# Optimization experiments

Hardware: AMD Instinct MI355X
Metric: run time of the kernel (lower is better)

Reference implementation:

```python
import jax, jax.numpy as jnp
import numpy as np

NEG_CAUSAL = -1e10  # matches torch buffer triu(ones*-1e10, diag=1)
NEG_PAD = -10000.0
NUM_HEADS = 16


def setup_inputs() -> dict:
    key = jax.random.key(0)
    ks = jax.random.split(key, 6)
    B, S, D = 2, 2048, 1024
    scale = 0.02
    return {
        "hidden_states": jax.random.normal(ks[0], (B, S, D), jnp.float32),
        "attention_mask": jnp.ones((B, S), jnp.float32),
        "Wq": jax.random.normal(ks[1], (D, D), jnp.float32) * scale,
        "bq": jnp.zeros((D,), jnp.float32),
        "Wk": jax.random.normal(ks[2], (D, D), jnp.float32) * scale,
        "bk": jnp.zeros((D,), jnp.float32),
        "Wv": jax.random.normal(ks[3], (D, D), jnp.float32) * scale,
        "bv": jnp.zeros((D,), jnp.float32),
        "Wo": jax.random.normal(ks[4], (D, D), jnp.float32) * scale,
        "bo": jnp.zeros((D,), jnp.float32),
    }


def reference(hidden_states, attention_mask, Wq, bq, Wk, bk, Wv, bv, Wo, bo):
    B, S, D = hidden_states.shape
    H = NUM_HEADS
    hd = D // H

    def heads(x):  # [B,S,D] -> [B,H,S,hd]
        return x.reshape(B, S, H, hd).transpose(0, 2, 1, 3)

    q = heads(hidden_states @ Wq + bq)
    k = heads(hidden_states @ Wk + bk)
    v = heads(hidden_states @ Wv + bv)

    scores = jnp.einsum("bhqd,bhkd->bhqk", q, k) / jnp.sqrt(jnp.float32(hd))
    causal = jnp.triu(jnp.full((S, S), NEG_CAUSAL, jnp.float32), k=1)
    scores = scores + causal
    # additive padding mask: (1 - m) * -10000, broadcast over heads and query pos
    scores = scores + (1.0 - attention_mask)[:, None, None, :] * NEG_PAD

    probs = jax.nn.softmax(scores, axis=-1)
    # dropout p=0.1 is inactive in eval mode (training=False)
    ctx = jnp.einsum("bhqk,bhkd->bhqd", probs, v)
    ctx = ctx.transpose(0, 2, 1, 3).reshape(B, S, D)
    return ctx @ Wo + bo
```

## Files before the change

### kernel.cpp

```cpp
#include <hip/hip_runtime.h>

typedef __attribute__((ext_vector_type(8))) short short8_t;
typedef __attribute__((ext_vector_type(4))) float float4_t;
typedef unsigned short u16;
typedef unsigned int u32;
typedef unsigned long long u64;

__device__ inline u16 f2bf(float x) {
  union { float f; u32 u; } v; v.f = x;
  u32 r = v.u + 0x7FFFu + ((v.u >> 16) & 1u);
  return (u16)(r >> 16);
}
#if __has_builtin(__builtin_amdgcn_cvt_pk_bf16_f32)
typedef __attribute__((ext_vector_type(2))) __bf16 bf162_t;
__device__ inline u32 pk2(float a, float b) {
  union { bf162_t v; u32 u; } cv;
  cv.v = __builtin_amdgcn_cvt_pk_bf16_f32(a, b);
  return cv.u;
}
#else
__device__ inline u32 pk2(float a, float b) {
  return (u32)f2bf(a) | ((u32)f2bf(b) << 16);
}
#endif

__global__ __launch_bounds__(256) void prologue(const float* __restrict__ X,
                                                const float* __restrict__ Wq, const float* __restrict__ Wk,
                                                const float* __restrict__ Wv, const float* __restrict__ Wo,
                                                u16* __restrict__ Xb, u16* __restrict__ WqkvT,
                                                u16* __restrict__ WoT, const float* __restrict__ maskp,
                                                u32* __restrict__ flags) {
  __shared__ float tls[32][33];
  int bid = blockIdx.x;
  if (bid < 4096) {
    int i = bid * 256 + threadIdx.x;
    float4_t x = ((const float4_t*)X)[i];
    union { u32 u[2]; u64 ll; } o;
    o.u[0] = pk2(x[0], x[1]);
    o.u[1] = pk2(x[2], x[3]);
    ((u64*)Xb)[i] = o.ll;
  } else if (bid < 8192) {
    int t = bid - 4096;
    int mat = t >> 10, tile = t & 1023;
    const float* W = (mat == 0) ? Wq : (mat == 1) ? Wk : (mat == 2) ? Wv : Wo;
    u16* WT = (mat < 3) ? WqkvT + ((size_t)mat << 20) : WoT;
    int tx = threadIdx.x & 31, ty = threadIdx.x >> 5;
    int c0 = (tile & 31) * 32, r0 = (tile >> 5) * 32;
    #pragma unroll
    for (int i = 0; i < 4; ++i)
      tls[ty + i * 8][tx] = W[(r0 + ty + i * 8) * 1024 + c0 + tx];
    __syncthreads();
    #pragma unroll
    for (int i = 0; i < 4; ++i)
      WT[(size_t)(c0 + ty + i * 8) * 1024 + r0 + tx] = f2bf(tls[tx][ty + i * 8]);
  } else {
    int b = bid - 8192;
    const float* mb = maskp + (b << 11) + threadIdx.x * 8;
    bool ok = true;
    #pragma unroll
    for (int i = 0; i < 8; ++i) ok &= (mb[i] == 1.0f);
    u64 bal = __ballot(ok);
    int w = threadIdx.x >> 6;
    if ((threadIdx.x & 63) == 0) tls[0][w] = (bal == ~0ull) ? 1.0f : 0.0f;
    __syncthreads();
    if (threadIdx.x == 0)
      flags[b] = (tls[0][0] != 0.0f && tls[0][1] != 0.0f &&
                  tls[0][2] != 0.0f && tls[0][3] != 0.0f) ? 1u : 0u;
  }
}

__global__ __launch_bounds__(256) void gemm128(const u16* __restrict__ A, const u16* __restrict__ BT,
                                               const float* __restrict__ bias0, const float* __restrict__ bias1,
                                               const float* __restrict__ bias2,
                                               void* __restrict__ o0, void* __restrict__ o1, void* __restrict__ o2) {
  __shared__ __align__(16) u16 Als[128 * 64];
  __shared__ __align__(16) u16 Bls[128 * 64];
  int g = blockIdx.x;
  int mh = g / 384, r = g - mh * 384;
  int n0t = r >> 4;
  int m0t = mh * 16 + (r & 15);
  const int m0 = m0t * 128, n0 = n0t * 128;
  const int lane = threadIdx.x & 63, wave = threadIdx.x >> 6;
  const int quad = lane >> 4, c = lane & 15;
  const int wm = wave >> 1, wn = wave & 1;

  const int srow = lane >> 3, schunk = lane & 7;
  int soff[4], dst[4];
  #pragma unroll
  for (int q = 0; q < 4; ++q) {
    int rr = wave * 32 + q * 8 + srow;
    soff[q] = rr * 1024 + (schunk << 3);
    dst[q]  = rr * 64 + ((schunk ^ (rr & 7)) << 3);
  }
  const u16* gA = A + (size_t)m0 * 1024;
  const u16* gB = BT + (size_t)n0 * 1024;

  int ar[2][4], br[2][4];
  #pragma unroll
  for (int ko = 0; ko < 2; ++ko) {
    #pragma unroll
    for (int i = 0; i < 4; ++i) {
      int rowa = wm * 64 + i * 16 + c;
      ar[ko][i] = rowa * 64 + (((ko * 4 + quad) ^ (rowa & 7)) << 3);
      int rowb = wn * 64 + i * 16 + c;
      br[ko][i] = rowb * 64 + (((ko * 4 + quad) ^ (rowb & 7)) << 3);
    }
  }

  short8_t ra[4], rb[4];
  #pragma unroll
  for (int q = 0; q < 4; ++q) ra[q] = *(const short8_t*)(gA + soff[q]);
  #pragma unroll
  for (int q = 0; q < 4; ++q) rb[q] = *(const short8_t*)(gB + soff[q]);

  float4_t acc[4][4] = {};
  for (int k0 = 0; k0 < 1024; k0 += 64) {
    #pragma unroll
    for (int q = 0; q < 4; ++q) *(short8_t*)&Als[dst[q]] = ra[q];
    #pragma unroll
    for (int q = 0; q < 4; ++q) *(short8_t*)&Bls[dst[q]] = rb[q];
    __syncthreads();
    if (k0 < 960) {
      #pragma unroll
      for (int q = 0; q < 4; ++q) ra[q] = *(const short8_t*)(gA + soff[q] + k0 + 64);
      #pragma unroll
      for (int q = 0; q < 4; ++q) rb[q] = *(const short8_t*)(gB + soff[q] + k0 + 64);
    }
    #pragma unroll
    for (int ko = 0; ko < 2; ++ko) {
      short8_t af[4], bfr[4];
      #pragma unroll
      for (int i = 0; i < 4; ++i) af[i] = *(const short8_t*)&Als[ar[ko][i]];
      #pragma unroll
      for (int j = 0; j < 4; ++j) bfr[j] = *(const short8_t*)&Bls[br[ko][j]];
      #pragma unroll
      for (int i = 0; i < 4; ++i)
        #pragma unroll
        for (int j = 0; j < 4; ++j)
          acc[i][j] = __builtin_amdgcn_mfma_f32_16x16x32_bf16(af[i], bfr[j], acc[i][j], 0, 0, 0);
    }
    __syncthreads();
  }

  const int mrow = m0 + wm * 64, ncol = n0 + wn * 64;
  #pragma unroll
  for (int j = 0; j < 4; ++j) {
    int colb = ncol + j * 16 + c;
    int which = colb >> 10;
    int n1 = colb & 1023, h = n1 >> 6, d = n1 & 63;
    const float* bp = (which == 0) ? bias0 : (which == 1 ? bias1 : bias2);
    float bv = bp[n1];
    #pragma unroll
    for (int i = 0; i < 4; ++i) {
      int rowb = mrow + i * 16 + quad * 4;
      int b = rowb >> 11, s = rowb & 2047;
      if (which == 2) {
        u16* o = (u16*)o2 + (((size_t)(b * 16 + h) * 64 + d) * 2048 + s);
        union { u32 u[2]; u64 ll; } ov;
        ov.u[0] = pk2(acc[i][j][0] + bv, acc[i][j][1] + bv);
        ov.u[1] = pk2(acc[i][j][2] + bv, acc[i][j][3] + bv);
        *(u64*)o = ov.ll;
      } else {
        float sc = (which == 0) ? 0.18033688011112042f : 1.0f;
        u16* o = (u16*)((which == 0) ? o0 : o1);
        #pragma unroll
        for (int rr = 0; rr < 4; ++rr)
          o[(((size_t)(b * 16 + h) * 2048 + (s + rr)) << 6) + d] = f2bf((acc[i][j][rr] + bv) * sc);
      }
    }
  }
}

__global__ __launch_bounds__(256) void gemm_oproj(const u16* __restrict__ A, const u16* __restrict__ BT,
                                                  const float* __restrict__ bias, float* __restrict__ o) {
  __shared__ __align__(16) u16 Als[64 * 64];
  __shared__ __align__(16) u16 Bls[128 * 64];
  int g = blockIdx.x;
  int m0t = g & 63, n0t = g >> 6;
  const int m0 = m0t * 64, n0 = n0t * 128;
  const int lane = threadIdx.x & 63, wave = threadIdx.x >> 6;
  const int quad = lane >> 4, c = lane & 15;

  const int srow = lane >> 3, schunk = lane & 7;
  int sA[2], dA[2], sB[4], dB[4];
  #pragma unroll
  for (int i = 0; i < 2; ++i) {
    int rr = wave * 16 + i * 8 + srow;
    sA[i] = rr * 1024 + (schunk << 3);
    dA[i] = rr * 64 + ((schunk ^ (rr & 7)) << 3);
  }
  #pragma unroll
  for (int q = 0; q < 4; ++q) {
    int rr = wave * 32 + q * 8 + srow;
    sB[q] = rr * 1024 + (schunk << 3);
    dB[q] = rr * 64 + ((schunk ^ (rr & 7)) << 3);
  }
  const u16* gA = A + (size_t)m0 * 1024;
  const u16* gB = BT + (size_t)n0 * 1024;

  int ar[2][4], br[2][2];
  #pragma unroll
  for (int ko = 0; ko < 2; ++ko) {
    #pragma unroll
    for (int i = 0; i < 4; ++i) {
      int rowa = i * 16 + c;
      ar[ko][i] = rowa * 64 + (((ko * 4 + quad) ^ (rowa & 7)) << 3);
    }
    #pragma unroll
    for (int j = 0; j < 2; ++j) {
      int rowb = wave * 32 + j * 16 + c;
      br[ko][j] = rowb * 64 + (((ko * 4 + quad) ^ (rowb & 7)) << 3);
    }
  }

  short8_t ra[2], rb[4];
  #pragma unroll
  for (int i = 0; i < 2; ++i) ra[i] = *(const short8_t*)(gA + sA[i]);
  #pragma unroll
  for (int q = 0; q < 4; ++q) rb[q] = *(const short8_t*)(gB + sB[q]);

  float4_t acc[4][2] = {};
  for (int k0 = 0; k0 < 1024; k0 += 64) {
    #pragma unroll
    for (int i = 0; i < 2; ++i) *(short8_t*)&Als[dA[i]] = ra[i];
    #pragma unroll
    for (int q = 0; q < 4; ++q) *(short8_t*)&Bls[dB[q]] = rb[q];
    __syncthreads();
    if (k0 < 960) {
      #pragma unroll
      for (int i = 0; i < 2; ++i) ra[i] = *(const short8_t*)(gA + sA[i] + k0 + 64);
      #pragma unroll
      for (int q = 0; q < 4; ++q) rb[q] = *(const short8_t*)(gB + sB[q] + k0 + 64);
    }
    #pragma unroll
    for (int ko = 0; ko < 2; ++ko) {
      short8_t af[4], bf2[2];
      #pragma unroll
      for (int i = 0; i < 4; ++i) af[i] = *(const short8_t*)&Als[ar[ko][i]];
      #pragma unroll
      for (int j = 0; j < 2; ++j) bf2[j] = *(const short8_t*)&Bls[br[ko][j]];
      #pragma unroll
      for (int i = 0; i < 4; ++i)
        #pragma unroll
        for (int j = 0; j < 2; ++j)
          acc[i][j] = __builtin_amdgcn_mfma_f32_16x16x32_bf16(af[i], bf2[j], acc[i][j], 0, 0, 0);
    }
    __syncthreads();
  }

  #pragma unroll
  for (int i = 0; i < 4; ++i) {
    #pragma unroll
    for (int j = 0; j < 2; ++j) {
      int colb = n0 + wave * 32 + j * 16 + c;
      float bv = bias[colb];
      int rowb = m0 + i * 16 + quad * 4;
      #pragma unroll
      for (int rr = 0; rr < 4; ++rr)
        o[(size_t)(rowb + rr) * 1024 + colb] = acc[i][j][rr] + bv;
    }
  }
}

__device__ inline short8_t p_to_b_swap(const float* p) {
  u32 a0 = pk2(p[0], p[1]), a1 = pk2(p[2], p[3]);
  u32 b0 = pk2(p[4], p[5]), b1 = pk2(p[6], p[7]);
  asm("v_permlane32_swap_b32 %0, %1" : "+v"(a0), "+v"(b0));
  asm("v_permlane32_swap_b32 %0, %1" : "+v"(a1), "+v"(b1));
  asm("v_permlane16_swap_b32 %0, %1" : "+v"(a0), "+v"(b0));
  asm("v_permlane16_swap_b32 %0, %1" : "+v"(a1), "+v"(b1));
  union { u32 u[4]; short8_t v; } pf;
  pf.u[0] = a0; pf.u[1] = a1; pf.u[2] = b0; pf.u[3] = b1;
  return pf.v;
}

__global__ __launch_bounds__(256, 4) void attn_kernel(const u16* __restrict__ Q, const u16* __restrict__ K,
                                                      const u16* __restrict__ VT, const float* __restrict__ mask,
                                                      const u32* __restrict__ flags, u16* __restrict__ ctx) {
  __shared__ __align__(16) u16 Kls[2 * 64 * 64];
  __shared__ __align__(16) u16 Vls[2 * 64 * 64];
  const float C1 = 10000.0f * 1.4426950408889634f;
  int w = threadIdx.x >> 6, lane = threadIdx.x & 63;
  int quad = lane >> 4, c = lane & 15;
  int g = blockIdx.x;
  int bh = (g & 7) * 4 + ((g >> 3) & 3);
  int u = g >> 5;
  int qt = (u < 16) ? (31 - u) : (u - 16);
  int b = bh >> 4, h = bh & 15;
  bool ones = flags && (flags[b] != 0);
  const u16* Kp = K + ((size_t)bh << 17);
  const u16* Vp = VT + ((size_t)bh << 17);
  const float* mp = mask + (b << 11);
  int q0 = qt * 64 + w * 16;

  const u16* Qp = Q + (((size_t)bh * 2048 + q0 + c) << 6) + quad * 8;
  short8_t qf0 = *(const short8_t*)(Qp);
  short8_t qf1 = *(const short8_t*)(Qp + 32);

  const int srow = lane >> 3, schunk = lane & 7;
  const u16* gK[2]; const u16* gV[2]; int dK[2], dV[2];
  #pragma unroll
  for (int i = 0; i < 2; ++i) {
    int R = w * 16 + i * 8 + srow;
    gK[i] = Kp + R * 64 + (schunk << 3);
    dK[i] = R * 64 + ((schunk ^ (R & 7)) << 3);
    gV[i] = Vp + (size_t)R * 2048 + (schunk << 3);
    dV[i] = R * 64 + ((schunk ^ (R & 7)) << 3);
  }

  int koff[4][2];
  #pragma unroll
  for (int kg = 0; kg < 4; ++kg) {
    int r = kg * 16 + c;
    #pragma unroll
    for (int ko = 0; ko < 2; ++ko)
      koff[kg][ko] = r * 64 + (((ko * 4 + quad) ^ (r & 7)) << 3);
  }
  int voff[4][2];
  #pragma unroll
  for (int dblk = 0; dblk < 4; ++dblk) {
    int d = dblk * 16 + c;
    #pragma unroll
    for (int kc = 0; kc < 2; ++kc)
      voff[dblk][kc] = d * 64 + (((kc * 4 + quad) ^ (d & 7)) << 3);
  }

  int ke[8];
  #pragma unroll
  for (int e = 0; e < 8; ++e) ke[e] = ((e >> 2) << 4) + quad * 4 + (e & 3);
  int thr = w * 16 + c;

  float4_t O[4] = {};
  float l = 0.0f;

  short8_t kreg[2], vreg[2];
  #pragma unroll
  for (int i = 0; i < 2; ++i) { kreg[i] = *(const short8_t*)(gK[i]); vreg[i] = *(const short8_t*)(gV[i]); }

  for (int t = 0; t <= qt; ++t) {
    int kb = t << 6;
    int bufo = (t & 1) << 12;
    #pragma unroll
    for (int i = 0; i < 2; ++i) *(short8_t*)&Kls[bufo + dK[i]] = kreg[i];
    #pragma unroll
    for (int i = 0; i < 2; ++i) *(short8_t*)&Vls[bufo + dV[i]] = vreg[i];
    __syncthreads();
    if (t < qt) {
      int kb2 = (t + 1) << 6;
      #pragma unroll
      for (int i = 0; i < 2; ++i) {
        kreg[i] = *(const short8_t*)(gK[i] + (size_t)kb2 * 64);
        vreg[i] = *(const short8_t*)(gV[i] + kb2);
      }
    }
    float4_t s[4];
    __builtin_amdgcn_s_setprio(1);
    #pragma unroll
    for (int kg = 0; kg < 4; ++kg) {
      short8_t k0 = *(const short8_t*)&Kls[bufo + koff[kg][0]];
      short8_t k1 = *(const short8_t*)&Kls[bufo + koff[kg][1]];
      float4_t a = {};
      a = __builtin_amdgcn_mfma_f32_16x16x32_bf16(k0, qf0, a, 0, 0, 0);
      a = __builtin_amdgcn_mfma_f32_16x16x32_bf16(k1, qf1, a, 0, 0, 0);
      s[kg] = a;
    }
    __builtin_amdgcn_s_setprio(0);
    float4_t mpl[4];
    if (!ones) {
      #pragma unroll
      for (int kg = 0; kg < 4; ++kg)
        mpl[kg] = (*(const float4_t*)(mp + kb + kg * 16 + quad * 4) - 1.0f) * C1;
    }
    bool diag = (t == qt);
    short8_t pf[2];
    #pragma unroll
    for (int kc = 0; kc < 2; ++kc) {
      float p[8];
      #pragma unroll
      for (int e = 0; e < 8; ++e) {
        int kg = kc * 2 + (e >> 2);
        p[e] = s[kg][e & 3];
        if (!ones) p[e] += mpl[kg][e & 3];
      }
      if (diag) {
        #pragma unroll
        for (int e = 0; e < 8; ++e) {
          int ko2 = kc * 32 + ke[e];
          p[e] = (ko2 > thr) ? -50.0f : p[e];
        }
      }
      #pragma unroll
      for (int e = 0; e < 8; ++e) {
        float pe = exp2f(p[e]);
        p[e] = pe;
        l += pe;
      }
      pf[kc] = p_to_b_swap(p);
    }
    __builtin_amdgcn_s_setprio(1);
    #pragma unroll
    for (int dblk = 0; dblk < 4; ++dblk) {
      #pragma unroll
      for (int kc = 0; kc < 2; ++kc) {
        short8_t vf = *(const short8_t*)&Vls[bufo + voff[dblk][kc]];
        O[dblk] = __builtin_amdgcn_mfma_f32_16x16x32_bf16(vf, pf[kc], O[dblk], 0, 0, 0);
      }
    }
    __builtin_amdgcn_s_setprio(0);
  }
  l += __shfl_xor(l, 16);
  l += __shfl_xor(l, 32);
  float rl = 1.0f / l;
  u16* op = ctx + ((size_t)(b * 2048 + q0 + c) * 1024 + h * 64 + quad * 4);
  #pragma unroll
  for (int dblk = 0; dblk < 4; ++dblk) {
    union { u32 uu[2]; u64 ll; } ov;
    ov.uu[0] = pk2(O[dblk][0] * rl, O[dblk][1] * rl);
    ov.uu[1] = pk2(O[dblk][2] * rl, O[dblk][3] * rl);
    *(u64*)(op + dblk * 16) = ov.ll;
  }
}

extern "C" void kernel_launch(void* const* d_in, const int* in_sizes, int n_in,
                              void* d_out, int out_size, void* d_ws, size_t ws_size,
                              hipStream_t stream) {
  const float* X    = (const float*)d_in[0];
  const float* mask = (const float*)d_in[1];
  const float* Wq   = (const float*)d_in[2];
  const float* bq   = (const float*)d_in[3];
  const float* Wk   = (const float*)d_in[4];
  const float* bk   = (const float*)d_in[5];
  const float* Wv   = (const float*)d_in[6];
  const float* bv   = (const float*)d_in[7];
  const float* Wo   = (const float*)d_in[8];
  const float* bo   = (const float*)d_in[9];

  char* w = (char*)d_ws;
  u16* Xb     = (u16*)(w);
  u16* WqkvT  = (u16*)(w + (8ull  << 20));
  u16* WoT    = (u16*)(w + (14ull << 20));
  u16* Qb     = (u16*)(w + (16ull << 20));
  u16* Kb     = (u16*)(w + (24ull << 20));
  u16* VTb    = (u16*)(w + (32ull << 20));
  u16* Ctx    = (u16*)(w + (40ull << 20));
  u32* flags  = (ws_size >= (48ull << 20) + 8) ? (u32*)(w + (48ull << 20)) : nullptr;

  prologue<<<flags ? 8194 : 8192, 256, 0, stream>>>(X, Wq, Wk, Wv, Wo, Xb, WqkvT, WoT, mask, flags);
  gemm128<<<768, 256, 0, stream>>>(Xb, WqkvT, bq, bk, bv, Qb, Kb, VTb);
  attn_kernel<<<1024, 256, 0, stream>>>(Qb, Kb, VTb, mask, flags, Ctx);
  gemm_oproj<<<512, 256, 0, stream>>>(Ctx, WoT, bo, (float*)d_out);
}
```

Measured before the change: 187.4 us.

## Fuse X bf16 conversion into QKV GEMM and enlarge O-proj tiles

The QKV GEMM now loads fp32 X directly and converts it to bf16 while staging into LDS, which removes the separate X conversion pass and its intermediate write and read. The output projection moves from 64x128 to 128x128 tiles using a 2x2 wave layout, which halves the block count and raises data reuse per block. In exchange, the QKV GEMM reads twice the A bytes from global memory and uses more registers for prefetch. The O-proj launch drops to 256 blocks, which may leave some CUs idle.

```diff
diff --git a/kernel.cpp b/kernel.cpp
--- a/kernel.cpp
+++ b/kernel.cpp
@@ -24,23 +24,14 @@
 }
 #endif
 
-__global__ __launch_bounds__(256) void prologue(const float* __restrict__ X,
-                                                const float* __restrict__ Wq, const float* __restrict__ Wk,
+__global__ __launch_bounds__(256) void prologue(const float* __restrict__ Wq, const float* __restrict__ Wk,
                                                 const float* __restrict__ Wv, const float* __restrict__ Wo,
-                                                u16* __restrict__ Xb, u16* __restrict__ WqkvT,
-                                                u16* __restrict__ WoT, const float* __restrict__ maskp,
-                                                u32* __restrict__ flags) {
+                                                u16* __restrict__ WqkvT, u16* __restrict__ WoT,
+                                                const float* __restrict__ maskp, u32* __restrict__ flags) {
   __shared__ float tls[32][33];
   int bid = blockIdx.x;
   if (bid < 4096) {
-    int i = bid * 256 + threadIdx.x;
-    float4_t x = ((const float4_t*)X)[i];
-    union { u32 u[2]; u64 ll; } o;
-    o.u[0] = pk2(x[0], x[1]);
-    o.u[1] = pk2(x[2], x[3]);
-    ((u64*)Xb)[i] = o.ll;
-  } else if (bid < 8192) {
-    int t = bid - 4096;
+    int t = bid;
     int mat = t >> 10, tile = t & 1023;
     const float* W = (mat == 0) ? Wq : (mat == 1) ? Wk : (mat == 2) ? Wv : Wo;
     u16* WT = (mat < 3) ? WqkvT + ((size_t)mat << 20) : WoT;
@@ -54,7 +45,7 @@
     for (int i = 0; i < 4; ++i)
       WT[(size_t)(c0 + ty + i * 8) * 1024 + r0 + tx] = f2bf(tls[tx][ty + i * 8]);
   } else {
-    int b = bid - 8192;
+    int b = bid - 4096;
     const float* mb = maskp + (b << 11) + threadIdx.x * 8;
     bool ok = true;
     #pragma unroll
@@ -69,10 +60,10 @@
   }
 }
 
-__global__ __launch_bounds__(256) void gemm128(const u16* __restrict__ A, const u16* __restrict__ BT,
-                                               const float* __restrict__ bias0, const float* __restrict__ bias1,
-                                               const float* __restrict__ bias2,
-                                               void* __restrict__ o0, void* __restrict__ o1, void* __restrict__ o2) {
+__global__ __launch_bounds__(256) void gemm_qkv(const float* __restrict__ X, const u16* __restrict__ BT,
+                                                const float* __restrict__ bias0, const float* __restrict__ bias1,
+                                                const float* __restrict__ bias2,
+                                                void* __restrict__ o0, void* __restrict__ o1, void* __restrict__ o2) {
   __shared__ __align__(16) u16 Als[128 * 64];
   __shared__ __align__(16) u16 Bls[128 * 64];
   int g = blockIdx.x;
@@ -92,7 +83,7 @@
     soff[q] = rr * 1024 + (schunk << 3);
     dst[q]  = rr * 64 + ((schunk ^ (rr & 7)) << 3);
   }
-  const u16* gA = A + (size_t)m0 * 1024;
+  const float* gA = X + (size_t)m0 * 1024;
   const u16* gB = BT + (size_t)n0 * 1024;
 
   int ar[2][4], br[2][4];
@@ -107,22 +98,36 @@
     }
   }
 
-  short8_t ra[4], rb[4];
-  #pragma unroll
-  for (int q = 0; q < 4; ++q) ra[q] = *(const short8_t*)(gA + soff[q]);
+  float4_t fa[4][2];
+  short8_t rb[4];
+  #pragma unroll
+  for (int q = 0; q < 4; ++q) {
+    fa[q][0] = *(const float4_t*)(gA + soff[q]);
+    fa[q][1] = *(const float4_t*)(gA + soff[q] + 4);
+  }
   #pragma unroll
   for (int q = 0; q < 4; ++q) rb[q] = *(const short8_t*)(gB + soff[q]);
 
   float4_t acc[4][4] = {};
   for (int k0 = 0; k0 < 1024; k0 += 64) {
     #pragma unroll
-    for (int q = 0; q < 4; ++q) *(short8_t*)&Als[dst[q]] = ra[q];
+    for (int q = 0; q < 4; ++q) {
+      union { u32 u[4]; short8_t v; } cv;
+      cv.u[0] = pk2(fa[q][0][0], fa[q][0][1]);
+      cv.u[1] = pk2(fa[q][0][2], fa[q][0][3]);
+      cv.u[2] = pk2(fa[q][1][0], fa[q][1][1]);
+      cv.u[3] = pk2(fa[q][1][2], fa[q][1][3]);
+      *(short8_t*)&Als[dst[q]] = cv.v;
+    }
     #pragma unroll
     for (int q = 0; q < 4; ++q) *(short8_t*)&Bls[dst[q]] = rb[q];
     __syncthreads();
     if (k0 < 960) {
       #pragma unroll
-      for (int q = 0; q < 4; ++q) ra[q] = *(const short8_t*)(gA + soff[q] + k0 + 64);
+      for (int q = 0; q < 4; ++q) {
+        fa[q][0] = *(const float4_t*)(gA + soff[q] + k0 + 64);
+        fa[q][1] = *(const float4_t*)(gA + soff[q] + k0 + 68);
+      }
       #pragma unroll
       for (int q = 0; q < 4; ++q) rb[q] = *(const short8_t*)(gB + soff[q] + k0 + 64);
     }
@@ -173,88 +178,81 @@
 
 __global__ __launch_bounds__(256) void gemm_oproj(const u16* __restrict__ A, const u16* __restrict__ BT,
                                                   const float* __restrict__ bias, float* __restrict__ o) {
-  __shared__ __align__(16) u16 Als[64 * 64];
+  __shared__ __align__(16) u16 Als[128 * 64];
   __shared__ __align__(16) u16 Bls[128 * 64];
   int g = blockIdx.x;
-  int m0t = g & 63, n0t = g >> 6;
-  const int m0 = m0t * 64, n0 = n0t * 128;
+  int m0t = g & 31, n0t = g >> 5;
+  const int m0 = m0t * 128, n0 = n0t * 128;
   const int lane = threadIdx.x & 63, wave = threadIdx.x >> 6;
   const int quad = lane >> 4, c = lane & 15;
+  const int wm = wave >> 1, wn = wave & 1;
 
   const int srow = lane >> 3, schunk = lane & 7;
-  int sA[2], dA[2], sB[4], dB[4];
-  #pragma unroll
-  for (int i = 0; i < 2; ++i) {
-    int rr = wave * 16 + i * 8 + srow;
-    sA[i] = rr * 1024 + (schunk << 3);
-    dA[i] = rr * 64 + ((schunk ^ (rr & 7)) << 3);
-  }
+  int soff[4], dst[4];
   #pragma unroll
   for (int q = 0; q < 4; ++q) {
     int rr = wave * 32 + q * 8 + srow;
-    sB[q] = rr * 1024 + (schunk << 3);
-    dB[q] = rr * 64 + ((schunk ^ (rr & 7)) << 3);
+    soff[q] = rr * 1024 + (schunk << 3);
+    dst[q]  = rr * 64 + ((schunk ^ (rr & 7)) << 3);
   }
   const u16* gA = A + (size_t)m0 * 1024;
   const u16* gB = BT + (size_t)n0 * 1024;
 
-  int ar[2][4], br[2][2];
+  int ar[2][4], br[2][4];
   #pragma unroll
   for (int ko = 0; ko < 2; ++ko) {
     #pragma unroll
     for (int i = 0; i < 4; ++i) {
-      int rowa = i * 16 + c;
+      int rowa = wm * 64 + i * 16 + c;
       ar[ko][i] = rowa * 64 + (((ko * 4 + quad) ^ (rowa & 7)) << 3);
-    }
-    #pragma unroll
-    for (int j = 0; j < 2; ++j) {
-      int rowb = wave * 32 + j * 16 + c;
-      br[ko][j] = rowb * 64 + (((ko * 4 + quad) ^ (rowb & 7)) << 3);
-    }
-  }
-
-  short8_t ra[2], rb[4];
-  #pragma unroll
-  for (int i = 0; i < 2; ++i) ra[i] = *(const short8_t*)(gA + sA[i]);
-  #pragma unroll
-  for (int q = 0; q < 4; ++q) rb[q] = *(const short8_t*)(gB + sB[q]);
-
-  float4_t acc[4][2] = {};
+      int rowb = wn * 64 + i * 16 + c;
+      br[ko][i] = rowb * 64 + (((ko * 4 + quad) ^ (rowb & 7)) << 3);
+    }
+  }
+
+  short8_t ra[4], rb[4];
+  #pragma unroll
+  for (int q = 0; q < 4; ++q) ra[q] = *(const short8_t*)(gA + soff[q]);
+  #pragma unroll
+  for (int q = 0; q < 4; ++q) rb[q] = *(const short8_t*)(gB + soff[q]);
+
+  float4_t acc[4][4] = {};
   for (int k0 = 0; k0 < 1024; k0 += 64) {
     #pragma unroll
-    for (int i = 0; i < 2; ++i) *(short8_t*)&Als[dA[i]] = ra[i];
-    #pragma unroll
-    for (int q = 0; q < 4; ++q) *(short8_t*)&Bls[dB[q]] = rb[q];
+    for (int q = 0; q < 4; ++q) *(short8_t*)&Als[dst[q]] = ra[q];
+    #pragma unroll
+    for (int q = 0; q < 4; ++q) *(short8_t*)&Bls[dst[q]] = rb[q];
     __syncthreads();
     if (k0 < 960) {
       #pragma unroll
-      for (int i = 0; i < 2; ++i) ra[i] = *(const short8_t*)(gA + sA[i] + k0 + 64);
-      #pragma unroll
-      for (int q = 0; q < 4; ++q) rb[q] = *(const short8_t*)(gB + sB[q] + k0 + 64);
+      for (int q = 0; q < 4; ++q) ra[q] = *(const short8_t*)(gA + soff[q] + k0 + 64);
+      #pragma unroll
+      for (int q = 0; q < 4; ++q) rb[q] = *(const short8_t*)(gB + soff[q] + k0 + 64);
     }
     #pragma unroll
     for (int ko = 0; ko < 2; ++ko) {
-      short8_t af[4], bf2[2];
+      short8_t af[4], bfr[4];
       #pragma unroll
       for (int i = 0; i < 4; ++i) af[i] = *(const short8_t*)&Als[ar[ko][i]];
       #pragma unroll
-      for (int j = 0; j < 2; ++j) bf2[j] = *(const short8_t*)&Bls[br[ko][j]];
+      for (int j = 0; j < 4; ++j) bfr[j] = *(const short8_t*)&Bls[br[ko][j]];
       #pragma unroll
       for (int i = 0; i < 4; ++i)
         #pragma unroll
-        for (int j = 0; j < 2; ++j)
-          acc[i][j] = __builtin_amdgcn_mfma_f32_16x16x32_bf16(af[i], bf2[j], acc[i][j], 0, 0, 0);
-    }
-    __syncthreads();
-  }
-
+        for (int j = 0; j < 4; ++j)
+          acc[i][j] = __builtin_amdgcn_mfma_f32_16x16x32_bf16(af[i], bfr[j], acc[i][j], 0, 0, 0);
+    }
+    __syncthreads();
+  }
+
+  const int mrow = m0 + wm * 64, ncol = n0 + wn * 64;
   #pragma unroll
   for (int i = 0; i < 4; ++i) {
     #pragma unroll
-    for (int j = 0; j < 2; ++j) {
-      int colb = n0 + wave * 32 + j * 16 + c;
+    for (int j = 0; j < 4; ++j) {
+      int colb = ncol + j * 16 + c;
       float bv = bias[colb];
-      int rowb = m0 + i * 16 + quad * 4;
+      int rowb = mrow + i * 16 + quad * 4;
       #pragma unroll
       for (int rr = 0; rr < 4; ++rr)
         o[(size_t)(rowb + rr) * 1024 + colb] = acc[i][j][rr] + bv;
@@ -436,7 +434,6 @@
   const float* bo   = (const float*)d_in[9];
 
   char* w = (char*)d_ws;
-  u16* Xb     = (u16*)(w);
   u16* WqkvT  = (u16*)(w + (8ull  << 20));
   u16* WoT    = (u16*)(w + (14ull << 20));
   u16* Qb     = (u16*)(w + (16ull << 20));
@@ -445,8 +442,8 @@
   u16* Ctx    = (u16*)(w + (40ull << 20));
   u32* flags  = (ws_size >= (48ull << 20) + 8) ? (u32*)(w + (48ull << 20)) : nullptr;
 
-  prologue<<<flags ? 8194 : 8192, 256, 0, stream>>>(X, Wq, Wk, Wv, Wo, Xb, WqkvT, WoT, mask, flags);
-  gemm128<<<768, 256, 0, stream>>>(Xb, WqkvT, bq, bk, bv, Qb, Kb, VTb);
+  prologue<<<flags ? 4098 : 4096, 256, 0, stream>>>(Wq, Wk, Wv, Wo, WqkvT, WoT, mask, flags);
+  gemm_qkv<<<768, 256, 0, stream>>>(X, WqkvT, bq, bk, bv, Qb, Kb, VTb);
   attn_kernel<<<1024, 256, 0, stream>>>(Qb, Kb, VTb, mask, flags, Ctx);
-  gemm_oproj<<<512, 256, 0, stream>>>(Ctx, WoT, bo, (float*)d_out);
-}
+  gemm_oproj<<<256, 256, 0, stream>>>(Ctx, WoT, bo, (float*)d_out);
+}
```

New measurement: 193.2 us. 1.03x slower.
